# Kernel optimization log

Hardware: AMD Instinct MI355X
Metric: run time of the kernel (lower is better)

## Reference

```python
import jax, jax.numpy as jnp
import numpy as np

D_MODEL = 1024
NUM_HEADS = 16
DEPTH = D_MODEL // NUM_HEADS
B, S = 2, 2048


def setup_inputs() -> dict:
    key = jax.random.key(0)
    ks = jax.random.split(key, 12)
    std = 1.0 / np.sqrt(D_MODEL)
    inp = {
        "q": jax.random.normal(ks[0], (B, S, D_MODEL), dtype=jnp.float32),
        "k": jax.random.normal(ks[1], (B, S, D_MODEL), dtype=jnp.float32),
        "v": jax.random.normal(ks[2], (B, S, D_MODEL), dtype=jnp.float32),
        "mask": jax.random.randint(ks[3], (B, 1, 1, S), 0, 2, dtype=jnp.int32),
        "wq": jax.random.normal(ks[4], (D_MODEL, D_MODEL), dtype=jnp.float32) * std,
        "bq": jnp.zeros((D_MODEL,), dtype=jnp.float32),
        "wk": jax.random.normal(ks[5], (D_MODEL, D_MODEL), dtype=jnp.float32) * std,
        "bk": jnp.zeros((D_MODEL,), dtype=jnp.float32),
        "wv": jax.random.normal(ks[6], (D_MODEL, D_MODEL), dtype=jnp.float32) * std,
        "bv": jnp.zeros((D_MODEL,), dtype=jnp.float32),
        "wo": jax.random.normal(ks[7], (D_MODEL, D_MODEL), dtype=jnp.float32) * std,
        "bo": jnp.zeros((D_MODEL,), dtype=jnp.float32),
    }
    return inp


def _split_heads(x):
    # (B, S, D) -> (B, H, S, depth)
    b, s, _ = x.shape
    return x.reshape(b, s, NUM_HEADS, DEPTH).transpose(0, 2, 1, 3)


def reference(q, k, v, mask, wq, bq, wk, bk, wv, bv, wo, bo):
    qh = _split_heads(q @ wq + bq)   # (B,H,S,depth)
    kh = _split_heads(k @ wk + bk)
    vh = _split_heads(v @ wv + bv)
    scale = 1.0 / jnp.sqrt(jnp.float32(DEPTH))
    logits = jnp.einsum("bhqd,bhkd->bhqk", qh, kh) * scale  # (B,H,Sq,Sk)
    logits = logits + mask.astype(logits.dtype) * -1e9
    attn = jax.nn.softmax(logits, axis=-1)
    out = jnp.einsum("bhqk,bhkd->bhqd", attn, vh)  # (B,H,Sq,depth)
    out = out.transpose(0, 2, 1, 3).reshape(q.shape[0], -1, D_MODEL)
    return out @ wo + bo
```

## Files before the change

### kernel.cpp

```cpp
#include <hip/hip_runtime.h>
#include <hip/hip_bf16.h>
#include <stdint.h>


typedef __bf16 bf16;
typedef __bf16 bf16x8 __attribute__((ext_vector_type(8)));
typedef __bf16 bf16x4 __attribute__((ext_vector_type(4)));
typedef float  f32x4  __attribute__((ext_vector_type(4)));

#define D_MODEL 1024
#define S_LEN   2048
#define NH      16
#define DEPTH   64

#define LOG2E   1.4426950408889634f
#define QSCALE  (0.125f * LOG2E)
#define SMAX    20.0f
#define PADPEN  (-30000.0f)

__device__ __forceinline__ void gload_lds16(const void* g, void* l) {
  __builtin_amdgcn_global_load_lds(
      (__attribute__((address_space(1))) void*)g,
      (__attribute__((address_space(3))) void*)l,
      16, 0, 0);
}

__global__ __launch_bounds__(256) void setup(
    const void* __restrict__ q, const void* __restrict__ k,
    const void* __restrict__ v, const int* __restrict__ mask,
    const void* __restrict__ wq, const void* __restrict__ wk,
    const void* __restrict__ wv, const void* __restrict__ wo,
    const void* __restrict__ bq, const void* __restrict__ bk,
    const void* __restrict__ bv, const void* __restrict__ bo,
    bf16* __restrict__ wqT, bf16* __restrict__ wkT,
    bf16* __restrict__ wvT, bf16* __restrict__ woT,
    bf16* __restrict__ bqb, bf16* __restrict__ bkb,
    bf16* __restrict__ bvb, bf16* __restrict__ bob,
    bf16* __restrict__ qb, bf16* __restrict__ kb, bf16* __restrict__ vb,
    int* __restrict__ cpos, int* __restrict__ nb, int* __restrict__ flagout)
{
  const int t = threadIdx.x;
  uint32_t w = ((const uint32_t*)q)[t];
  uint32_t e = (w >> 7) & 0xFF;
  int inr = (e >= 90 && e <= 150) ? 1 : 0;
  __shared__ int flg;
  int cnt = __syncthreads_count(inr);
  if (t == 0) flg = (cnt > 160) ? 1 : 0;
  __syncthreads();
  int flag = flg;

  const int bid = blockIdx.x;
  if (bid < 2) {
    const int b = bid;
    const int lane = t & 63, wv4 = t >> 6;
    __shared__ int wsum[4];
    int vals[8], s = 0;
#pragma unroll
    for (int j = 0; j < 8; ++j) {
      vals[j] = (mask[b * S_LEN + t * 8 + j] == 0) ? 1 : 0;
      s += vals[j];
    }
    int acc = s;
    for (int off = 1; off < 64; off <<= 1) {
      int u = __shfl_up(acc, off);
      if (lane >= off) acc += u;
    }
    if (lane == 63) wsum[wv4] = acc;
    __syncthreads();
    int base = 0;
    for (int w4 = 0; w4 < 4; ++w4) base += (w4 < wv4) ? wsum[w4] : 0;
    int ex = base + acc - s;
#pragma unroll
    for (int j = 0; j < 8; ++j) {
      cpos[b * S_LEN + t * 8 + j] = vals[j] ? ex : -1;
      ex += vals[j];
    }
    if (t == 255) nb[b] = base + acc;
    if (b == 0 && t == 0) *flagout = flag;
  } else if (bid < 6) {
    const int j = bid - 2;
    const void* B; bf16* O;
    switch (j) {
      case 0:  B = bq; O = bqb; break;
      case 1:  B = bk; O = bkb; break;
      case 2:  B = bv; O = bvb; break;
      default: B = bo; O = bob; break;
    }
    const float sc = (j == 0) ? QSCALE : 1.0f;
    for (int jj = 0; jj < 4; ++jj) {
      const int i = t + jj * 256;
      const float val = flag ? (float)((const bf16*)B)[i] : ((const float*)B)[i];
      O[i] = (bf16)(val * sc);
    }
  } else if (bid < 6 + 4096) {
    const int job = bid - 6;
    const int wsel = job >> 10, rem = job & 1023;
    const void* W; bf16* T;
    switch (wsel) {
      case 0:  W = wq; T = wqT; break;
      case 1:  W = wk; T = wkT; break;
      case 2:  W = wv; T = wvT; break;
      default: W = wo; T = woT; break;
    }
    const float sc = (wsel == 0) ? QSCALE : 1.0f;
    __shared__ float tile[32][33];
    const int tx = t & 31, ty = t >> 5;
    const int x0 = (rem & 31) * 32;
    const int y0 = (rem >> 5) * 32;
    for (int i = ty; i < 32; i += 8) {
      const size_t gi = (size_t)(y0 + i) * D_MODEL + x0 + tx;
      tile[i][tx] = flag ? (float)((const bf16*)W)[gi] : ((const float*)W)[gi];
    }
    __syncthreads();
    for (int i = ty; i < 32; i += 8)
      T[(size_t)(x0 + i) * D_MODEL + y0 + tx] = (bf16)(tile[tx][i] * sc);
  } else {
    if (flag) return;
    const int job = bid - 4102;
    const int tensor = job >> 11, blk = job & 2047;
    const void* src; bf16* dst;
    switch (tensor) {
      case 0:  src = q; dst = qb; break;
      case 1:  src = k; dst = kb; break;
      default: src = v; dst = vb; break;
    }
    const size_t idx = ((size_t)blk * 256 + t) * 8;
    const float* s = (const float*)src + idx;
    f32x4 a = *(const f32x4*)(s);
    f32x4 b2 = *(const f32x4*)(s + 4);
    bf16x8 o;
    for (int i = 0; i < 4; ++i) { o[i] = (bf16)a[i]; o[4 + i] = (bf16)b2[i]; }
    *(bf16x8*)(dst + idx) = o;
  }
}

struct GArgs {
  const bf16* A;
  const void* Araw;
  const bf16* BT;
  const bf16* bias;
  void* out;
  const int* cpos;
  int mode;
};

__device__ __forceinline__ void gemm_body(const GArgs& g, int flag)
{
  const bf16* A = flag ? (const bf16*)g.Araw : g.A;

  __shared__ __align__(16) bf16 As[128 * 32];
  __shared__ __align__(16) bf16 Bs[128 * 32];
  const int tid  = threadIdx.x;
  const int wave = tid >> 6, lane = tid & 63;
  const int quad = lane >> 4, l16 = lane & 15;

  const int flat = blockIdx.y * 8 + blockIdx.x;
  const int xcd = flat & 7, pos = flat >> 3;
  const int bx = (xcd & 1) * 4 + (pos & 3);
  const int by = (xcd >> 1) * 8 + (pos >> 2);
  const int m0 = by * 128, n0 = bx * 128;

  const int wm = (wave >> 1) * 64, wn = (wave & 1) * 64;
  const int srow = lane >> 2;
  const int scol = (lane & 3) * 8;

  f32x4 acc[4][4] = {};

  const bf16* Ag = A    + (size_t)(m0 + wave * 32 + srow) * D_MODEL + scol;
  const bf16* Bg = g.BT + (size_t)(n0 + wave * 32 + srow) * D_MODEL + scol;
  bf16* Asw = As + (wave * 32) * 32;
  bf16* Bsw = Bs + (wave * 32) * 32;

  for (int kt = 0; kt < D_MODEL; kt += 32) {
    __syncthreads();
    gload_lds16(Ag + kt,                Asw);
    gload_lds16(Ag + kt + 16 * D_MODEL, Asw + 16 * 32);
    gload_lds16(Bg + kt,                Bsw);
    gload_lds16(Bg + kt + 16 * D_MODEL, Bsw + 16 * 32);
    __syncthreads();

    bf16x8 af[4], bfv[4];
#pragma unroll
    for (int mi = 0; mi < 4; ++mi)
      af[mi] = *(const bf16x8*)(As + (wm + mi * 16 + l16) * 32 + quad * 8);
#pragma unroll
    for (int ni = 0; ni < 4; ++ni)
      bfv[ni] = *(const bf16x8*)(Bs + (wn + ni * 16 + l16) * 32 + quad * 8);
#pragma unroll
    for (int mi = 0; mi < 4; ++mi)
#pragma unroll
      for (int ni = 0; ni < 4; ++ni)
        acc[mi][ni] = __builtin_amdgcn_mfma_f32_16x16x32_bf16(
            af[mi], bfv[ni], acc[mi][ni], 0, 0, 0);
  }

#pragma unroll
  for (int mi = 0; mi < 4; ++mi) {
    const int row0 = m0 + wm + mi * 16 + quad * 4;
    const int b = row0 >> 11, s = row0 & 2047;
    int cp[4];
    if (g.mode >= 2) {
#pragma unroll
      for (int r = 0; r < 4; ++r) cp[r] = g.cpos[b * S_LEN + s + r];
    }
#pragma unroll
    for (int ni = 0; ni < 4; ++ni) {
      const int col  = n0 + wn + ni * 16 + l16;
      const float bv = (float)g.bias[col];
      const int hh = col >> 6, d = col & 63;
      if (g.mode == 3) {
        bf16* base = (bf16*)g.out + (size_t)(b * NH + hh) * S_LEN * DEPTH + d;
#pragma unroll
        for (int r = 0; r < 4; ++r)
          if (cp[r] >= 0) base[(size_t)cp[r] * DEPTH] = (bf16)(acc[mi][ni][r] + bv);
      } else if (g.mode == 2) {
        bf16* base = (bf16*)g.out + ((size_t)(b * NH + hh) * DEPTH + d) * S_LEN;
#pragma unroll
        for (int r = 0; r < 4; ++r)
          if (cp[r] >= 0) base[cp[r]] = (bf16)(acc[mi][ni][r] + bv);
      } else if (g.mode == 1) {
        bf16* op = (bf16*)g.out + ((size_t)(b * NH + hh) * S_LEN + s) * DEPTH + d;
#pragma unroll
        for (int r = 0; r < 4; ++r)
          op[(size_t)r * DEPTH] = (bf16)(acc[mi][ni][r] + bv);
      } else {
        if (flag) {
          bf16* op = (bf16*)g.out + (size_t)row0 * D_MODEL + col;
#pragma unroll
          for (int r = 0; r < 4; ++r)
            op[(size_t)r * D_MODEL] = (bf16)(acc[mi][ni][r] + bv);
        } else {
          float* op = (float*)g.out + (size_t)row0 * D_MODEL + col;
#pragma unroll
          for (int r = 0; r < 4; ++r)
            op[(size_t)r * D_MODEL] = acc[mi][ni][r] + bv;
        }
      }
    }
  }
}

__global__ __launch_bounds__(256) void gemm_qkv(GArgs g0, GArgs g1, GArgs g2,
                                                const int* __restrict__ flagp)
{
  const GArgs& g = (blockIdx.z == 0) ? g0 : ((blockIdx.z == 1) ? g1 : g2);
  gemm_body(g, *flagp);
}

__global__ __launch_bounds__(256) void gemm_out(GArgs g,
                                                const int* __restrict__ flagp)
{
  gemm_body(g, *flagp);
}

__global__ __launch_bounds__(256) void attn(
    const bf16* __restrict__ Qh, const bf16* __restrict__ Kc,
    const bf16* __restrict__ Vc, const int* __restrict__ nbp,
    bf16* __restrict__ Oh)
{
  const int bh = blockIdx.y;
  const int b  = bh >> 4;
  const int h  = bh & 15;
  const int q0 = blockIdx.x * 128;
  const int tid = threadIdx.x, wave = tid >> 6, lane = tid & 63;
  const int quad = lane >> 4, l16 = lane & 15;

  __shared__ __align__(16) bf16 Ks[64][72];
  __shared__ __align__(16) bf16 Vts[64][72];
  __shared__ __align__(16) bf16 Ps[4][32][72];

  const int nbv = nbp[b];
  const int nb_pad = (nbv + 63) & ~63;

  const bf16* Qg = Qh + ((size_t)bh * S_LEN + q0 + wave * 32) * DEPTH;
  bf16x8 aq00 = *(const bf16x8*)(Qg + (size_t)l16 * DEPTH + quad * 8);
  bf16x8 aq01 = *(const bf16x8*)(Qg + (size_t)l16 * DEPTH + 32 + quad * 8);
  bf16x8 aq10 = *(const bf16x8*)(Qg + (size_t)(16 + l16) * DEPTH + quad * 8);
  bf16x8 aq11 = *(const bf16x8*)(Qg + (size_t)(16 + l16) * DEPTH + 32 + quad * 8);

  bf16x8 ones;
#pragma unroll
  for (int j = 0; j < 8; ++j) ones[j] = (bf16)1.0f;

  f32x4 o_acc[2][4] = {};
  f32x4 l_acc[2] = {};

  const bf16* Kg = Kc + (size_t)bh * S_LEN * DEPTH;
  const bf16* Vg = Vc + (size_t)bh * DEPTH * S_LEN;

  const int sr0 = tid >> 3, sc0 = (tid & 7) * 8;
  const int sr1 = sr0 + 32;

  bf16x8 kr0, kr1, vr0, vr1;
  {
    kr0 = *(const bf16x8*)(Kg + (size_t)sr0 * DEPTH + sc0);
    kr1 = *(const bf16x8*)(Kg + (size_t)sr1 * DEPTH + sc0);
    vr0 = *(const bf16x8*)(Vg + (size_t)sr0 * S_LEN + sc0);
    vr1 = *(const bf16x8*)(Vg + (size_t)sr1 * S_LEN + sc0);
  }

  for (int kb = 0; kb < nb_pad; kb += 64) {
    __syncthreads();
    *(bf16x8*)(&Ks[sr0][sc0])  = kr0;
    *(bf16x8*)(&Ks[sr1][sc0])  = kr1;
    *(bf16x8*)(&Vts[sr0][sc0]) = vr0;
    *(bf16x8*)(&Vts[sr1][sc0]) = vr1;
    __syncthreads();
    if (kb + 64 < nb_pad) {
      kr0 = *(const bf16x8*)(Kg + (size_t)(kb + 64 + sr0) * DEPTH + sc0);
      kr1 = *(const bf16x8*)(Kg + (size_t)(kb + 64 + sr1) * DEPTH + sc0);
      vr0 = *(const bf16x8*)(Vg + (size_t)sr0 * S_LEN + kb + 64 + sc0);
      vr1 = *(const bf16x8*)(Vg + (size_t)sr1 * S_LEN + kb + 64 + sc0);
    }

    f32x4 sacc[2][4] = {};
#pragma unroll
    for (int jn = 0; jn < 4; ++jn) {
      bf16x8 bk0 = *(const bf16x8*)(&Ks[jn * 16 + l16][quad * 8]);
      bf16x8 bk1 = *(const bf16x8*)(&Ks[jn * 16 + l16][32 + quad * 8]);
      sacc[0][jn] = __builtin_amdgcn_mfma_f32_16x16x32_bf16(aq00, bk0, sacc[0][jn], 0, 0, 0);
      sacc[0][jn] = __builtin_amdgcn_mfma_f32_16x16x32_bf16(aq01, bk1, sacc[0][jn], 0, 0, 0);
      sacc[1][jn] = __builtin_amdgcn_mfma_f32_16x16x32_bf16(aq10, bk0, sacc[1][jn], 0, 0, 0);
      sacc[1][jn] = __builtin_amdgcn_mfma_f32_16x16x32_bf16(aq11, bk1, sacc[1][jn], 0, 0, 0);
    }

#pragma unroll
    for (int jn = 0; jn < 4; ++jn) {
      const int key = kb + jn * 16 + l16;
      const float pen = (key < nbv) ? (-SMAX) : PADPEN;
#pragma unroll
      for (int qs = 0; qs < 2; ++qs)
#pragma unroll
        for (int r = 0; r < 4; ++r)
          Ps[wave][qs * 16 + quad * 4 + r][jn * 16 + l16] =
              (bf16)__builtin_amdgcn_exp2f(sacc[qs][jn][r] + pen);
    }

    bf16x8 ap00 = *(const bf16x8*)(&Ps[wave][l16][quad * 8]);
    bf16x8 ap01 = *(const bf16x8*)(&Ps[wave][l16][32 + quad * 8]);
    bf16x8 ap10 = *(const bf16x8*)(&Ps[wave][16 + l16][quad * 8]);
    bf16x8 ap11 = *(const bf16x8*)(&Ps[wave][16 + l16][32 + quad * 8]);
#pragma unroll
    for (int jd = 0; jd < 4; ++jd) {
      bf16x8 bv0 = *(const bf16x8*)(&Vts[jd * 16 + l16][quad * 8]);
      bf16x8 bv1 = *(const bf16x8*)(&Vts[jd * 16 + l16][32 + quad * 8]);
      o_acc[0][jd] = __builtin_amdgcn_mfma_f32_16x16x32_bf16(ap00, bv0, o_acc[0][jd], 0, 0, 0);
      o_acc[0][jd] = __builtin_amdgcn_mfma_f32_16x16x32_bf16(ap01, bv1, o_acc[0][jd], 0, 0, 0);
      o_acc[1][jd] = __builtin_amdgcn_mfma_f32_16x16x32_bf16(ap10, bv0, o_acc[1][jd], 0, 0, 0);
      o_acc[1][jd] = __builtin_amdgcn_mfma_f32_16x16x32_bf16(ap11, bv1, o_acc[1][jd], 0, 0, 0);
    }
    l_acc[0] = __builtin_amdgcn_mfma_f32_16x16x32_bf16(ap00, ones, l_acc[0], 0, 0, 0);
    l_acc[0] = __builtin_amdgcn_mfma_f32_16x16x32_bf16(ap01, ones, l_acc[0], 0, 0, 0);
    l_acc[1] = __builtin_amdgcn_mfma_f32_16x16x32_bf16(ap10, ones, l_acc[1], 0, 0, 0);
    l_acc[1] = __builtin_amdgcn_mfma_f32_16x16x32_bf16(ap11, ones, l_acc[1], 0, 0, 0);
  }

#pragma unroll
  for (int qs = 0; qs < 2; ++qs) {
#pragma unroll
    for (int r = 0; r < 4; ++r) {
      const int s = q0 + wave * 32 + qs * 16 + quad * 4 + r;
      const float inv = 1.f / l_acc[qs][r];
#pragma unroll
      for (int jd = 0; jd < 4; ++jd) {
        const int d = jd * 16 + l16;
        Oh[(size_t)(b * S_LEN + s) * D_MODEL + h * DEPTH + d] =
            (bf16)(o_acc[qs][jd][r] * inv);
      }
    }
  }
}

extern "C" void kernel_launch(void* const* d_in, const int* in_sizes, int n_in,
                              void* d_out, int out_size, void* d_ws, size_t ws_size,
                              hipStream_t stream)
{
  const void* q    = d_in[0];
  const void* k    = d_in[1];
  const void* v    = d_in[2];
  const int*  mask = (const int*)d_in[3];
  const void* wq   = d_in[4];
  const void* bq   = d_in[5];
  const void* wk   = d_in[6];
  const void* bk   = d_in[7];
  const void* wv   = d_in[8];
  const void* bv   = d_in[9];
  const void* wo   = d_in[10];
  const void* bo   = d_in[11];

  char* ws = (char*)d_ws;
  const size_t MB = 1u << 20;
  bf16* Qh  = (bf16*)(ws + 0 * MB);
  bf16* Kc  = (bf16*)(ws + 8 * MB);
  bf16* Vc  = (bf16*)(ws + 16 * MB);
  bf16* Oh  = (bf16*)(ws + 24 * MB);
  bf16* wqT = (bf16*)(ws + 32 * MB);
  bf16* wkT = (bf16*)(ws + 34 * MB);
  bf16* wvT = (bf16*)(ws + 36 * MB);
  bf16* woT = (bf16*)(ws + 38 * MB);
  bf16* bqb = (bf16*)(ws + 40 * MB);
  bf16* bkb = (bf16*)(ws + 40 * MB + 4096);
  bf16* bvb = (bf16*)(ws + 40 * MB + 8192);
  bf16* bob = (bf16*)(ws + 40 * MB + 12288);
  int*  flag = (int*)(ws + 40 * MB + 32768);
  int*  cpos = (int*)(ws + 40 * MB + 65536);
  int*  nb   = (int*)(ws + 40 * MB + 65536 + 16384);
  bf16* qb  = (bf16*)(ws + 41 * MB);
  bf16* kb_ = (bf16*)(ws + 49 * MB);
  bf16* vb_ = (bf16*)(ws + 57 * MB);

  setup<<<10246, 256, 0, stream>>>(
      q, k, v, mask, wq, wk, wv, wo, bq, bk, bv, bo,
      wqT, wkT, wvT, woT, bqb, bkb, bvb, bob,
      qb, kb_, vb_, cpos, nb, flag);

  GArgs gq{qb,  q,  wqT, bqb, Qh, nullptr, 1};
  GArgs gk{kb_, k,  wkT, bkb, Kc, cpos,    3};
  GArgs gv{vb_, v,  wvT, bvb, Vc, cpos,    2};
  gemm_qkv<<<dim3(8, 32, 3), 256, 0, stream>>>(gq, gk, gv, flag);

  attn<<<dim3(16, 32), 256, 0, stream>>>(Qh, Kc, Vc, nb, Oh);

  GArgs go{Oh, Oh, woT, bob, d_out, nullptr, 0};
  gemm_out<<<dim3(8, 32), 256, 0, stream>>>(go, flag);
}
```

Measured before the change: 228.1 us.

## Double-buffer GEMM LDS tiles and XOR-swizzle columns to avoid bank conflicts

The projection GEMM now keeps two LDS buffers. It issues the global-to-LDS loads for the next k-tile before computing on the current one, so memory latency overlaps with the MFMA work and one of the two barriers per iteration goes away. It also applies an XOR swizzle to the 16-byte column chunks on both the store and read side, to reduce LDS bank conflicts on the fragment reads. LDS use doubles, which may lower occupancy. With a single barrier per iteration, correctness depends on the async LDS loads completing before the barrier.

```diff
diff --git a/kernel.cpp b/kernel.cpp
--- a/kernel.cpp
+++ b/kernel.cpp
@@ -148,8 +148,8 @@
 {
   const bf16* A = flag ? (const bf16*)g.Araw : g.A;
 
-  __shared__ __align__(16) bf16 As[128 * 32];
-  __shared__ __align__(16) bf16 Bs[128 * 32];
+  __shared__ __align__(16) bf16 As[2][128 * 32];
+  __shared__ __align__(16) bf16 Bs[2][128 * 32];
   const int tid  = threadIdx.x;
   const int wave = tid >> 6, lane = tid & 63;
   const int quad = lane >> 4, l16 = lane & 15;
@@ -162,36 +162,46 @@
 
   const int wm = (wave >> 1) * 64, wn = (wave & 1) * 64;
   const int srow = lane >> 2;
-  const int scol = (lane & 3) * 8;
+  const int scol = (((lane & 3) ^ ((lane >> 3) & 3)) * 8);
 
   f32x4 acc[4][4] = {};
 
   const bf16* Ag = A    + (size_t)(m0 + wave * 32 + srow) * D_MODEL + scol;
   const bf16* Bg = g.BT + (size_t)(n0 + wave * 32 + srow) * D_MODEL + scol;
-  bf16* Asw = As + (wave * 32) * 32;
-  bf16* Bsw = Bs + (wave * 32) * 32;
-
-  for (int kt = 0; kt < D_MODEL; kt += 32) {
-    __syncthreads();
-    gload_lds16(Ag + kt,                Asw);
-    gload_lds16(Ag + kt + 16 * D_MODEL, Asw + 16 * 32);
-    gload_lds16(Bg + kt,                Bsw);
-    gload_lds16(Bg + kt + 16 * D_MODEL, Bsw + 16 * 32);
-    __syncthreads();
+  const int lbase = (wave * 32) * 32;
+  const int rsw = (quad ^ ((l16 >> 1) & 3)) * 8;
+
+  gload_lds16(Ag,                &As[0][lbase]);
+  gload_lds16(Ag + 16 * D_MODEL, &As[0][lbase + 16 * 32]);
+  gload_lds16(Bg,                &Bs[0][lbase]);
+  gload_lds16(Bg + 16 * D_MODEL, &Bs[0][lbase + 16 * 32]);
+  __syncthreads();
+
+  int cur = 0;
+  for (int kt = 0; kt < D_MODEL; kt += 32, cur ^= 1) {
+    if (kt + 32 < D_MODEL) {
+      const int nxt = cur ^ 1;
+      gload_lds16(Ag + kt + 32,                &As[nxt][lbase]);
+      gload_lds16(Ag + kt + 32 + 16 * D_MODEL, &As[nxt][lbase + 16 * 32]);
+      gload_lds16(Bg + kt + 32,                &Bs[nxt][lbase]);
+      gload_lds16(Bg + kt + 32 + 16 * D_MODEL, &Bs[nxt][lbase + 16 * 32]);
+    }
 
     bf16x8 af[4], bfv[4];
 #pragma unroll
     for (int mi = 0; mi < 4; ++mi)
-      af[mi] = *(const bf16x8*)(As + (wm + mi * 16 + l16) * 32 + quad * 8);
+      af[mi] = *(const bf16x8*)(&As[cur][(wm + mi * 16 + l16) * 32 + rsw]);
 #pragma unroll
     for (int ni = 0; ni < 4; ++ni)
-      bfv[ni] = *(const bf16x8*)(Bs + (wn + ni * 16 + l16) * 32 + quad * 8);
+      bfv[ni] = *(const bf16x8*)(&Bs[cur][(wn + ni * 16 + l16) * 32 + rsw]);
 #pragma unroll
     for (int mi = 0; mi < 4; ++mi)
 #pragma unroll
       for (int ni = 0; ni < 4; ++ni)
         acc[mi][ni] = __builtin_amdgcn_mfma_f32_16x16x32_bf16(
             af[mi], bfv[ni], acc[mi][ni], 0, 0, 0);
+
+    __syncthreads();
   }
 
 #pragma unroll
```

Result: no change. 232.0 us (+1.7%).
